# Optimization experiments

Hardware: AMD Instinct MI355X
Metric: run time of the kernel (lower is better)

The kernel has to match this reference:

```python
import jax, jax.numpy as jnp
import numpy as np
from jax import lax

H = W = 1024

def _conv_sig(x, w, b):
    # 3x3 conv, padding=1 (SAME), NCHW / OIHW, followed by sigmoid
    y = lax.conv_general_dilated(x, w, (1, 1), 'SAME',
                                 dimension_numbers=('NCHW', 'OIHW', 'NCHW'))
    return jax.nn.sigmoid(y + b[None, :, None, None])


def setup_inputs() -> dict:
    key = jax.random.key(0)
    ks = jax.random.split(key, 20)
    d = {
        'x':  jax.random.normal(ks[0], (1, 3, H, W), jnp.float32),
        'x2': jax.random.normal(ks[1], (1, 3, H, W), jnp.float32),
        'w1a': jax.random.normal(ks[2], (1, 3, 3, 3), jnp.float32) * 0.1,
        'b1a': jax.random.normal(ks[3], (1,), jnp.float32) * 0.1,
        'w2a': jax.random.normal(ks[4], (1, 4, 3, 3), jnp.float32) * 0.1,
        'b2a': jax.random.normal(ks[5], (1,), jnp.float32) * 0.1,
        'w3a': jax.random.normal(ks[6], (1, 5, 3, 3), jnp.float32) * 0.1,
        'b3a': jax.random.normal(ks[7], (1,), jnp.float32) * 0.1,
        'w1b': jax.random.normal(ks[8], (1, 3, 3, 3), jnp.float32) * 0.1,
        'b1b': jax.random.normal(ks[9], (1,), jnp.float32) * 0.1,
        'w2b': jax.random.normal(ks[10], (1, 4, 3, 3), jnp.float32) * 0.1,
        'b2b': jax.random.normal(ks[11], (1,), jnp.float32) * 0.1,
        'w3b': jax.random.normal(ks[12], (1, 5, 3, 3), jnp.float32) * 0.1,
        'b3b': jax.random.normal(ks[13], (1,), jnp.float32) * 0.1,
        'lw1': jax.random.normal(ks[14], (128, 6), jnp.float32) * 0.1,
        'lb1': jax.random.normal(ks[15], (128,), jnp.float32) * 0.1,
        'lw2': jax.random.normal(ks[16], (2, 128), jnp.float32) * 0.1,
        'lb2': jax.random.normal(ks[17], (2,), jnp.float32) * 0.1,
    }
    return d


def _encode(x, params):
    # three stacked conv(3x3)+sigmoid blocks with densenet-style concat: C 3->4->5->6
    (w1, b1), (w2, b2), (w3, b3) = params
    x = jnp.concatenate([x, _conv_sig(x, w1, b1)], axis=1)
    x = jnp.concatenate([x, _conv_sig(x, w2, b2)], axis=1)
    x = jnp.concatenate([x, _conv_sig(x, w3, b3)], axis=1)
    return x  # [1, 6, H, W]


def reference(x, x2, w1a, b1a, w2a, b2a, w3a, b3a,
              w1b, b1b, w2b, b2b, w3b, b3b, lw1, lb1, lw2, lb2):
    # name branch: passthrough (3-channel input, e.g. name='opt')
    xa = _encode(x,  [(w1a, b1a), (w2a, b2a), (w3a, b3a)])
    xb = _encode(x2, [(w1b, b1b), (w2b, b2b), (w3b, b3b)])
    x3 = xa - xb                                   # [1, 6, H, W]
    feat = jnp.transpose(x3, (0, 2, 3, 1)).reshape(H * W, 6)
    feat = feat @ lw1.T + lb1                      # [HW, 128]
    outfeature = feat @ lw2.T + lb2                # [HW, 2]
    den_x1 = jnp.transpose(xa, (0, 2, 3, 1)).reshape(H, W, 6)
    den_x2 = jnp.transpose(xb, (0, 2, 3, 1)).reshape(H, W, 6)
    return outfeature, den_x1, den_x2
```

## Files before the change

kernel.cpp:

```cpp
#include <hip/hip_runtime.h>

#define IMG  1024
#define TS   32
#define XTW  40
#define XTH  38
#define XTA  (XTH*XTW)
#define SG   36
#define S2G  34
#define OUT1 (2*IMG*IMG)
#define OUT2 (OUT1 + 6*IMG*IMG)

__device__ __forceinline__ float sigf(float y) { return 1.0f / (1.0f + __expf(-y)); }

__global__ __launch_bounds__(256, 4)
void unet_fused(const float* __restrict__ x, const float* __restrict__ x2,
                const float* __restrict__ w1a, const float* __restrict__ b1a,
                const float* __restrict__ w2a, const float* __restrict__ b2a,
                const float* __restrict__ w3a, const float* __restrict__ b3a,
                const float* __restrict__ w1b, const float* __restrict__ b1b,
                const float* __restrict__ w2b, const float* __restrict__ b2b,
                const float* __restrict__ w3b, const float* __restrict__ b3b,
                const float* __restrict__ lw1, const float* __restrict__ lb1,
                const float* __restrict__ lw2, const float* __restrict__ lb2,
                float* __restrict__ out)
{
    __shared__ float xt[3][XTA];
    __shared__ float s1[SG * SG];
    __shared__ float a2b[SG * SG];
    __shared__ float a3b[SG * SG];
    __shared__ float s2[S2G * S2G];
    __shared__ float wc[14];

    const int tid = threadIdx.x;

    int lin = blockIdx.y * gridDim.x + blockIdx.x;
    int nid = (lin & 7) * 128 + (lin >> 3);
    int bx = nid & 31, by = nid >> 5;
    const int R0 = by * TS, C0 = bx * TS;
    const bool edge = (bx == 0) | (bx == 31) | (by == 0) | (by == 31);

    if (tid < 12) {
        int o = tid / 6, ch = tid - o * 6;
        float acc = 0.0f;
        for (int k = 0; k < 128; ++k) acc += lw2[o * 128 + k] * lw1[k * 6 + ch];
        wc[tid] = acc;
    } else if (tid < 14) {
        int o = tid - 12;
        float acc = lb2[o];
        for (int k = 0; k < 128; ++k) acc += lw2[o * 128 + k] * lb1[k];
        wc[tid] = acc;
    }

    const float* XS[2] = {x, x2};
    const float* W1[2] = {w1a, w1b};
    const float* W2[2] = {w2a, w2b};
    const float* W3[2] = {w3a, w3b};
    const float* B1[2] = {b1a, b1b};
    const float* B2[2] = {b2a, b2b};
    const float* B3[2] = {b3a, b3b};

    float pa[4][2];

#pragma unroll
    for (int br = 0; br < 2; ++br) {
        __syncthreads();
        const float* xin = XS[br];
        if (!edge) {
            for (int it = tid; it < 3 * XTH * 10; it += 256) {
                int ch = it / (XTH * 10); int rem = it - ch * (XTH * 10);
                int row = rem / 10, seg = rem - row * 10;
                float4 v = *(const float4*)(xin + ch * (IMG * IMG) + (R0 - 3 + row) * IMG + (C0 - 4) + seg * 4);
                *(float4*)(&xt[ch][row * XTW + seg * 4]) = v;
            }
        } else {
            for (int it = tid; it < 3 * XTA; it += 256) {
                int ch = it / XTA; int rem = it - ch * XTA;
                int row = rem / XTW, col = rem - row * XTW;
                int gr = R0 - 3 + row, gc = C0 - 4 + col;
                float v = 0.0f;
                if ((unsigned)gr < (unsigned)IMG && (unsigned)gc < (unsigned)IMG)
                    v = xin[ch * (IMG * IMG) + gr * IMG + gc];
                xt[ch][rem] = v;
            }
        }
        __syncthreads();

        const float b1v = B1[br][0], b2v = B2[br][0], b3v = B3[br][0];

        if (tid < 216) {
            int strip = tid / 36, sc = tid - strip * 36;
            int r0 = strip * 6;
            float acc1[6], acc2[6], acc3[6];
#pragma unroll
            for (int q = 0; q < 6; ++q) { acc1[q] = b1v; acc2[q] = b2v; acc3[q] = b3v; }
            for (int ch = 0; ch < 3; ++ch) {
                float u9[9], v9[9], w9[9];
#pragma unroll
                for (int i = 0; i < 9; ++i) {
                    u9[i] = W1[br][ch * 9 + i];
                    v9[i] = W2[br][ch * 9 + i];
                    w9[i] = W3[br][ch * 9 + i];
                }
                const float* xp = &xt[ch][r0 * XTW + sc + 1];
#pragma unroll
                for (int rr = 0; rr < 8; ++rr) {
                    float a0 = xp[0], a1 = xp[1], a2v = xp[2];
                    xp += XTW;
#pragma unroll
                    for (int dy = 0; dy < 3; ++dy) {
                        int q = rr - dy;
                        if (q >= 0 && q < 6) {
                            acc1[q] += u9[dy * 3] * a0 + u9[dy * 3 + 1] * a1 + u9[dy * 3 + 2] * a2v;
                            acc2[q] += v9[dy * 3] * a0 + v9[dy * 3 + 1] * a1 + v9[dy * 3 + 2] * a2v;
                            acc3[q] += w9[dy * 3] * a0 + w9[dy * 3 + 1] * a1 + w9[dy * 3 + 2] * a2v;
                        }
                    }
                }
            }
            int gcol = C0 - 2 + sc;
            bool cok = (unsigned)gcol < (unsigned)IMG;
            int grow0 = R0 - 2 + r0;
#pragma unroll
            for (int q = 0; q < 6; ++q) {
                bool ok = cok && ((unsigned)(grow0 + q) < (unsigned)IMG);
                int o = (r0 + q) * SG + sc;
                s1[o]  = ok ? sigf(acc1[q]) : 0.0f;
                a2b[o] = acc2[q];
                a3b[o] = acc3[q];
            }
        }
        __syncthreads();

        if (tid < 204) {
            int strip = tid / 34, sc = tid - strip * 34;
            int r0 = strip * 6;
            float acc[6];
#pragma unroll
            for (int q = 0; q < 6; ++q) {
                int ar = r0 + q + 1; if (ar > 35) ar = 35;
                acc[q] = a2b[ar * SG + sc + 1];
            }
            float w9[9];
#pragma unroll
            for (int i = 0; i < 9; ++i) w9[i] = W2[br][27 + i];
#pragma unroll
            for (int rr = 0; rr < 8; ++rr) {
                int srow = r0 + rr; if (srow > 35) srow = 35;
                const float* p = &s1[srow * SG + sc];
                float a0 = p[0], a1 = p[1], a2v = p[2];
#pragma unroll
                for (int dy = 0; dy < 3; ++dy) {
                    int q = rr - dy;
                    if (q >= 0 && q < 6)
                        acc[q] += w9[dy * 3] * a0 + w9[dy * 3 + 1] * a1 + w9[dy * 3 + 2] * a2v;
                }
            }
            int gcol = C0 - 1 + sc;
            bool cok = (unsigned)gcol < (unsigned)IMG;
            int grow0 = R0 - 1 + r0;
#pragma unroll
            for (int q = 0; q < 6; ++q) {
                int sr = r0 + q;
                if (sr < S2G) {
                    bool ok = cok && ((unsigned)(grow0 + q) < (unsigned)IMG);
                    s2[sr * S2G + sc] = ok ? sigf(acc[q]) : 0.0f;
                }
            }
        }
        __syncthreads();

        {
            const int c = tid & 31, rs = tid >> 5;
            const int r0 = rs * 4;
            float acc[4], c1[4], c2[4];
#pragma unroll
            for (int q = 0; q < 4; ++q) acc[q] = a3b[(r0 + q + 2) * SG + (c + 2)];
            {
                float w9[9];
#pragma unroll
                for (int i = 0; i < 9; ++i) w9[i] = W3[br][27 + i];
                const float* p = &s1[(r0 + 1) * SG + (c + 1)];
#pragma unroll
                for (int rr = 0; rr < 6; ++rr) {
                    float a0 = p[0], a1 = p[1], a2v = p[2];
                    p += SG;
                    if (rr >= 1 && rr <= 4) c1[rr - 1] = a1;
#pragma unroll
                    for (int dy = 0; dy < 3; ++dy) {
                        int q = rr - dy;
                        if (q >= 0 && q < 4)
                            acc[q] += w9[dy * 3] * a0 + w9[dy * 3 + 1] * a1 + w9[dy * 3 + 2] * a2v;
                    }
                }
            }
            {
                float w9[9];
#pragma unroll
                for (int i = 0; i < 9; ++i) w9[i] = W3[br][36 + i];
                const float* p = &s2[r0 * S2G + c];
#pragma unroll
                for (int rr = 0; rr < 6; ++rr) {
                    float a0 = p[0], a1 = p[1], a2v = p[2];
                    p += S2G;
                    if (rr >= 1 && rr <= 4) c2[rr - 1] = a1;
#pragma unroll
                    for (int dy = 0; dy < 3; ++dy) {
                        int q = rr - dy;
                        if (q >= 0 && q < 4)
                            acc[q] += w9[dy * 3] * a0 + w9[dy * 3 + 1] * a1 + w9[dy * 3 + 2] * a2v;
                    }
                }
            }

            const int denOff = (br == 0) ? OUT1 : OUT2;
#pragma unroll
            for (int q = 0; q < 4; ++q) {
                float cur[6];
#pragma unroll
                for (int ch = 0; ch < 3; ++ch)
                    cur[ch] = xt[ch][(r0 + q + 3) * XTW + (c + 4)];
                cur[3] = c1[q];
                cur[4] = c2[q];
                cur[5] = sigf(acc[q]);

                int pix = (R0 + r0 + q) * IMG + C0 + c;
                float* pd = out + denOff + pix * 6;
#pragma unroll
                for (int ch = 0; ch < 6; ++ch) pd[ch] = cur[ch];

                if (br == 0) {
                    float p0 = 0.0f, p1 = 0.0f;
#pragma unroll
                    for (int ch = 0; ch < 6; ++ch) {
                        p0 += wc[ch]     * cur[ch];
                        p1 += wc[6 + ch] * cur[ch];
                    }
                    pa[q][0] = p0; pa[q][1] = p1;
                } else {
                    float o0 = pa[q][0] + wc[12];
                    float o1 = pa[q][1] + wc[13];
#pragma unroll
                    for (int ch = 0; ch < 6; ++ch) {
                        o0 -= wc[ch]     * cur[ch];
                        o1 -= wc[6 + ch] * cur[ch];
                    }
                    out[pix * 2]     = o0;
                    out[pix * 2 + 1] = o1;
                }
            }
        }
    }
}

extern "C" void kernel_launch(void* const* d_in, const int* in_sizes, int n_in,
                              void* d_out, int out_size, void* d_ws, size_t ws_size,
                              hipStream_t stream) {
    const float* x   = (const float*)d_in[0];
    const float* x2  = (const float*)d_in[1];
    const float* w1a = (const float*)d_in[2];
    const float* b1a = (const float*)d_in[3];
    const float* w2a = (const float*)d_in[4];
    const float* b2a = (const float*)d_in[5];
    const float* w3a = (const float*)d_in[6];
    const float* b3a = (const float*)d_in[7];
    const float* w1b = (const float*)d_in[8];
    const float* b1b = (const float*)d_in[9];
    const float* w2b = (const float*)d_in[10];
    const float* b2b = (const float*)d_in[11];
    const float* w3b = (const float*)d_in[12];
    const float* b3b = (const float*)d_in[13];
    const float* lw1 = (const float*)d_in[14];
    const float* lb1 = (const float*)d_in[15];
    const float* lw2 = (const float*)d_in[16];
    const float* lb2 = (const float*)d_in[17];
    float* out = (float*)d_out;

    dim3 grid(IMG / TS, IMG / TS);
    unet_fused<<<grid, 256, 0, stream>>>(x, x2,
                                         w1a, b1a, w2a, b2a, w3a, b3a,
                                         w1b, b1b, w2b, b2b, w3b, b3b,
                                         lw1, lb1, lw2, lb2, out);
}
```

Baseline: 163.3 us.

## Prefetch both branch input tiles into registers up front, drop block swizzle

Interior blocks now load the x and x2 halo tiles into registers at kernel start and later copy each branch's tile from registers into shared memory, so the second branch's global loads are issued early and can overlap the first branch's compute. The block-index swizzle is removed in favour of plain 2D block ordering, and the final output is written as a single float2 store. Holding ten float4 values in registers raises register pressure, which could lower occupancy under the 256x4 launch bound, and dropping the swizzle changes the order in which tiles are scheduled.

Measured after the change: 171.0 us. 1.05x slower.

```diff
diff --git a/kernel.cpp b/kernel.cpp
--- a/kernel.cpp
+++ b/kernel.cpp
@@ -5,6 +5,7 @@
 #define XTW  40
 #define XTH  38
 #define XTA  (XTH*XTW)
+#define NSEG (3*XTH*10)
 #define SG   36
 #define S2G  34
 #define OUT1 (2*IMG*IMG)
@@ -33,9 +34,7 @@
 
     const int tid = threadIdx.x;
 
-    int lin = blockIdx.y * gridDim.x + blockIdx.x;
-    int nid = (lin & 7) * 128 + (lin >> 3);
-    int bx = nid & 31, by = nid >> 5;
+    const int bx = blockIdx.x, by = blockIdx.y;
     const int R0 = by * TS, C0 = bx * TS;
     const bool edge = (bx == 0) | (bx == 31) | (by == 0) | (by == 31);
 
@@ -59,20 +58,37 @@
     const float* B2[2] = {b2a, b2b};
     const float* B3[2] = {b3a, b3b};
 
-    float pa[4][2];
-
-#pragma unroll
-    for (int br = 0; br < 2; ++br) {
-        __syncthreads();
-        const float* xin = XS[br];
-        if (!edge) {
-            for (int it = tid; it < 3 * XTH * 10; it += 256) {
+    float4 h[2][5];
+    int hoff[5];
+    if (!edge) {
+#pragma unroll
+        for (int k = 0; k < 5; ++k) {
+            int it = tid + k * 256;
+            if (it < NSEG) {
                 int ch = it / (XTH * 10); int rem = it - ch * (XTH * 10);
                 int row = rem / 10, seg = rem - row * 10;
-                float4 v = *(const float4*)(xin + ch * (IMG * IMG) + (R0 - 3 + row) * IMG + (C0 - 4) + seg * 4);
-                *(float4*)(&xt[ch][row * XTW + seg * 4]) = v;
+                int g = ch * (IMG * IMG) + (R0 - 3 + row) * IMG + (C0 - 4) + seg * 4;
+                h[0][k] = *(const float4*)(x  + g);
+                h[1][k] = *(const float4*)(x2 + g);
+                hoff[k] = ch * XTA + row * XTW + seg * 4;
+            }
+        }
+    }
+
+    float pa[4][2];
+
+#pragma unroll
+    for (int br = 0; br < 2; ++br) {
+        __syncthreads();
+        if (!edge) {
+#pragma unroll
+            for (int k = 0; k < 5; ++k) {
+                int it = tid + k * 256;
+                if (it < NSEG)
+                    *(float4*)(&xt[0][hoff[k]]) = h[br][k];
             }
         } else {
+            const float* xin = XS[br];
             for (int it = tid; it < 3 * XTA; it += 256) {
                 int ch = it / XTA; int rem = it - ch * XTA;
                 int row = rem / XTW, col = rem - row * XTW;
@@ -244,8 +260,7 @@
                         o0 -= wc[ch]     * cur[ch];
                         o1 -= wc[6 + ch] * cur[ch];
                     }
-                    out[pix * 2]     = o0;
-                    out[pix * 2 + 1] = o1;
+                    *(float2*)(out + pix * 2) = make_float2(o0, o1);
                 }
             }
         }
```
